# Optimization experiments

Measured on AMD Instinct MI355X. Metric: run time of the kernel, lower is better.

The kernel has to match this reference:

```python
import jax, jax.numpy as jnp
import numpy as np

HEAD_DIM = 128
PATCH = (1, 2, 2)
MAX_SEQ = 1024
THETA = 10000.0
FIXED_REF = 30
H_DIM = 2 * (HEAD_DIM // 6)          # 42
W_DIM = 2 * (HEAD_DIM // 6)          # 42
T_DIM = HEAD_DIM - H_DIM - W_DIM     # 44


def _rope_1d(dim, max_seq_len, theta):
    # matches get_1d_rotary_pos_embed(use_real=True, repeat_interleave_real=True)
    inv = 1.0 / (theta ** (jnp.arange(0, dim, 2, dtype=jnp.float32) / dim))  # [dim/2]
    ang = jnp.arange(max_seq_len, dtype=jnp.float32)[:, None] * inv[None, :]  # [S, dim/2]
    cos = jnp.repeat(jnp.cos(ang), 2, axis=1)  # [S, dim]
    sin = jnp.repeat(jnp.sin(ang), 2, axis=1)
    return cos, sin


def setup_inputs() -> dict:
    key = jax.random.key(0)
    hs = jax.random.normal(key, (1, 16, 22, 120, 120), dtype=jnp.float32)
    t_cos, t_sin = _rope_1d(T_DIM, MAX_SEQ, THETA)
    h_cos, h_sin = _rope_1d(H_DIM, MAX_SEQ, THETA)
    w_cos, w_sin = _rope_1d(W_DIM, MAX_SEQ, THETA)
    return {
        "hidden_states": hs,
        "freq_t_cos": t_cos, "freq_h_cos": h_cos, "freq_w_cos": w_cos,
        "freq_t_sin": t_sin, "freq_h_sin": h_sin, "freq_w_sin": w_sin,
        "num_video_frames": 21,
        "num_ref_frames": 1,
    }


def _build(t_tab, h_tab, w_tab, pos_t, height, width):
    F = pos_t.shape[0]
    t = t_tab[pos_t]                 # [F, T_DIM]
    h = h_tab[:height]               # [height, H_DIM]
    w = w_tab[:width]                # [width, W_DIM]
    grid = jnp.concatenate([
        jnp.broadcast_to(t[:, None, None, :], (F, height, width, T_DIM)),
        jnp.broadcast_to(h[None, :, None, :], (F, height, width, H_DIM)),
        jnp.broadcast_to(w[None, None, :, :], (F, height, width, W_DIM)),
    ], axis=-1)                      # [F, height, width, HEAD_DIM]
    return grid.reshape(1, F * height * width, 1, HEAD_DIM)


def reference(hidden_states, freq_t_cos, freq_h_cos, freq_w_cos,
              freq_t_sin, freq_h_sin, freq_w_sin,
              num_video_frames, num_ref_frames):
    _, _, _, H, W = hidden_states.shape
    p_t, p_h, p_w = PATCH
    height, width = H // p_h, W // p_w
    video_pp = num_video_frames // p_t
    ref_pp = num_ref_frames // p_t
    # temporal positions: sequential for video frames, fixed 30 for ref frames
    pos_t = jnp.concatenate([
        jnp.arange(video_pp, dtype=jnp.int32),
        jnp.full((ref_pp,), FIXED_REF, dtype=jnp.int32),
    ])
    freqs_cos = _build(freq_t_cos, freq_h_cos, freq_w_cos, pos_t, height, width)
    freqs_sin = _build(freq_t_sin, freq_h_sin, freq_w_sin, pos_t, height, width)
    return freqs_cos, freqs_sin
```

## Files before the change

kernel.cpp:

```cpp
#include <hip/hip_runtime.h>


#define RP_T_DIM 44
#define RP_H_DIM 42
#define RP_W_DIM 42
#define RP_HEAD 128
#define RP_GH 60
#define RP_GW 60
#define RP_FIXED_REF 30
#define RP_TH 86
#define RP_TH_PAD 88
#define RP_WROW 44
#define RP_LDS_FLOATS (RP_TH_PAD + RP_GW * RP_WROW)

#define RP_BLOCK 320

__global__ __launch_bounds__(RP_BLOCK) void wan_rope_kernel(
    const float* __restrict__ t_cos, const float* __restrict__ h_cos,
    const float* __restrict__ w_cos, const float* __restrict__ t_sin,
    const float* __restrict__ h_sin, const float* __restrict__ w_sin,
    const int* __restrict__ nvf_ptr,
    float* __restrict__ out, long long sin_offset)
{
    __shared__ __align__(16) float lds_c[RP_LDS_FLOATS];
    __shared__ __align__(16) float lds_s[RP_LDS_FLOATS];

    const int tid = threadIdx.x;
    const int y = blockIdx.x;
    const int f = blockIdx.y;

    const int vpp = nvf_ptr[0];
    const int pos = (f < vpp) ? f : RP_FIXED_REF;

    if (tid < RP_T_DIM) {
        lds_c[tid] = t_cos[pos * RP_T_DIM + tid];
        lds_s[tid] = t_sin[pos * RP_T_DIM + tid];
    } else if (tid < RP_TH) {
        const int j = tid - RP_T_DIM;
        lds_c[tid] = h_cos[y * RP_H_DIM + j];
        lds_s[tid] = h_sin[y * RP_H_DIM + j];
    }

    for (int i = tid; i < 2 * RP_GW; i += RP_BLOCK) {
        const int x = i >> 1, j = i & 1;
        lds_c[RP_TH_PAD + x * RP_WROW + j] = h_cos[y * RP_H_DIM + 40 + j];
        lds_s[RP_TH_PAD + x * RP_WROW + j] = h_sin[y * RP_H_DIM + 40 + j];
    }

    for (int sIdx = tid; sIdx < RP_GW * RP_W_DIM; sIdx += RP_BLOCK) {
        const int x = sIdx / RP_W_DIM;
        const int j = sIdx - x * RP_W_DIM;
        lds_c[RP_TH_PAD + x * RP_WROW + 2 + j] = w_cos[sIdx];
        lds_s[RP_TH_PAD + x * RP_WROW + 2 + j] = w_sin[sIdx];
    }

    __syncthreads();

    const long long rowbase = (long long)f * (RP_GH * RP_GW) + y * RP_GW;
#pragma unroll
    for (int it = 0; it < 6; ++it) {
        const int flat = it * RP_BLOCK + tid;
        const int x = flat >> 5;
        const int q = flat & 31;
        const int lidx = (q < 21) ? (q << 2)
                                  : (RP_TH_PAD + x * RP_WROW + ((q - 21) << 2));
        const float4 c = *(const float4*)(lds_c + lidx);
        const float4 s = *(const float4*)(lds_s + lidx);
        const long long base = (rowbase + x) * RP_HEAD + (q << 2);
        *(float4*)(out + base) = c;
        *(float4*)(out + sin_offset + base) = s;
    }
}

extern "C" void kernel_launch(void* const* d_in, const int* in_sizes, int n_in,
                              void* d_out, int out_size, void* d_ws, size_t ws_size,
                              hipStream_t stream) {
    const float* t_cos = (const float*)d_in[1];
    const float* h_cos = (const float*)d_in[2];
    const float* w_cos = (const float*)d_in[3];
    const float* t_sin = (const float*)d_in[4];
    const float* h_sin = (const float*)d_in[5];
    const float* w_sin = (const float*)d_in[6];
    const int*   nvf   = (const int*)d_in[7];
    float* out = (float*)d_out;

    const long long per_out = (long long)out_size / 2;
    const int F = (int)(per_out / ((long long)RP_GH * RP_GW * RP_HEAD));

    dim3 block(RP_BLOCK);
    dim3 grid(RP_GH, F);
    wan_rope_kernel<<<grid, block, 0, stream>>>(
        t_cos, h_cos, w_cos, t_sin, h_sin, w_sin, nvf, out, per_out);
}
```

Measured before the change: 111.4 us.

## Process four frames per block to reuse staged width tables in LDS

Each block now handles up to four frames for one row instead of one, so the width cos/sin tables staged in shared memory are loaded once and reused across frames. The LDS layout is reorganised into separate regions for per-frame t rows, the shared h row and the w rows, and the store loop precomputes offsets and uses 32-bit indexing. The aim is to cut redundant global loads and per-block setup relative to the write-bound output stream. In exchange the grid has a quarter as many blocks, which may reduce parallelism, and the switch to int offsets assumes the output stays under 2^31 elements.

```diff
diff --git a/kernel.cpp b/kernel.cpp
--- a/kernel.cpp
+++ b/kernel.cpp
@@ -8,67 +8,79 @@
 #define RP_GH 60
 #define RP_GW 60
 #define RP_FIXED_REF 30
-#define RP_TH 86
-#define RP_TH_PAD 88
-#define RP_WROW 44
-#define RP_LDS_FLOATS (RP_TH_PAD + RP_GW * RP_WROW)
+#define RP_FPB 4
+#define RP_BLOCK 320
 
-#define RP_BLOCK 320
+#define RP_HB 176
+#define RP_WB 224
+#define RP_LDSF (RP_WB + RP_GW * 44)
 
 __global__ __launch_bounds__(RP_BLOCK) void wan_rope_kernel(
     const float* __restrict__ t_cos, const float* __restrict__ h_cos,
     const float* __restrict__ w_cos, const float* __restrict__ t_sin,
     const float* __restrict__ h_sin, const float* __restrict__ w_sin,
     const int* __restrict__ nvf_ptr,
-    float* __restrict__ out, long long sin_offset)
+    float* __restrict__ out, int sin_offset, int F)
 {
-    __shared__ __align__(16) float lds_c[RP_LDS_FLOATS];
-    __shared__ __align__(16) float lds_s[RP_LDS_FLOATS];
+    __shared__ __align__(16) float lds_c[RP_LDSF];
+    __shared__ __align__(16) float lds_s[RP_LDSF];
 
     const int tid = threadIdx.x;
-    const int y = blockIdx.x;
-    const int f = blockIdx.y;
+    const int y  = blockIdx.x;
+    const int f0 = blockIdx.y * RP_FPB;
+    const int nf = min(RP_FPB, F - f0);
+    const int vpp = nvf_ptr[0];
 
-    const int vpp = nvf_ptr[0];
-    const int pos = (f < vpp) ? f : RP_FIXED_REF;
-
-    if (tid < RP_T_DIM) {
-        lds_c[tid] = t_cos[pos * RP_T_DIM + tid];
-        lds_s[tid] = t_sin[pos * RP_T_DIM + tid];
-    } else if (tid < RP_TH) {
-        const int j = tid - RP_T_DIM;
-        lds_c[tid] = h_cos[y * RP_H_DIM + j];
-        lds_s[tid] = h_sin[y * RP_H_DIM + j];
+    if (tid < nf * RP_T_DIM) {
+        const int fl = tid / RP_T_DIM;
+        const int d  = tid - fl * RP_T_DIM;
+        const int ff = f0 + fl;
+        const int pos = (ff < vpp) ? ff : RP_FIXED_REF;
+        lds_c[tid] = t_cos[pos * RP_T_DIM + d];
+        lds_s[tid] = t_sin[pos * RP_T_DIM + d];
     }
-
-    for (int i = tid; i < 2 * RP_GW; i += RP_BLOCK) {
-        const int x = i >> 1, j = i & 1;
-        lds_c[RP_TH_PAD + x * RP_WROW + j] = h_cos[y * RP_H_DIM + 40 + j];
-        lds_s[RP_TH_PAD + x * RP_WROW + j] = h_sin[y * RP_H_DIM + 40 + j];
+    if (tid < RP_H_DIM) {
+        lds_c[RP_HB + tid] = h_cos[y * RP_H_DIM + tid];
+        lds_s[RP_HB + tid] = h_sin[y * RP_H_DIM + tid];
     }
-
-    for (int sIdx = tid; sIdx < RP_GW * RP_W_DIM; sIdx += RP_BLOCK) {
-        const int x = sIdx / RP_W_DIM;
-        const int j = sIdx - x * RP_W_DIM;
-        lds_c[RP_TH_PAD + x * RP_WROW + 2 + j] = w_cos[sIdx];
-        lds_s[RP_TH_PAD + x * RP_WROW + 2 + j] = w_sin[sIdx];
+    if (tid < 2 * RP_GW) {
+        const int x = tid >> 1, j = tid & 1;
+        lds_c[RP_WB + x * 44 + j] = h_cos[y * RP_H_DIM + 40 + j];
+        lds_s[RP_WB + x * 44 + j] = h_sin[y * RP_H_DIM + 40 + j];
     }
-
+    for (int i = tid; i < RP_GW * RP_W_DIM; i += RP_BLOCK) {
+        const int x = i / RP_W_DIM;
+        const int j = i - x * RP_W_DIM;
+        lds_c[RP_WB + x * 44 + 2 + j] = w_cos[i];
+        lds_s[RP_WB + x * 44 + 2 + j] = w_sin[i];
+    }
     __syncthreads();
 
-    const long long rowbase = (long long)f * (RP_GH * RP_GW) + y * RP_GW;
+    const int q  = tid & 31;
+    const int xb = tid >> 5;
+
+    const bool is_t = q < 11;
+    const int lidx0 = is_t ? (q << 2)
+                    : ((q < 21) ? (132 + (q << 2))
+                                : (140 + 44 * xb + (q << 2)));
+    const int finc = is_t ? RP_T_DIM : 0;
+    const int winc = (q >= 21) ? 440 : 0;
+
+    int base_f = (f0 * (RP_GH * RP_GW) + y * RP_GW + xb) * RP_HEAD + (q << 2);
+
+    for (int fl = 0; fl < nf; ++fl) {
+        int lidx = lidx0 + fl * finc;
+        int base = base_f;
 #pragma unroll
-    for (int it = 0; it < 6; ++it) {
-        const int flat = it * RP_BLOCK + tid;
-        const int x = flat >> 5;
-        const int q = flat & 31;
-        const int lidx = (q < 21) ? (q << 2)
-                                  : (RP_TH_PAD + x * RP_WROW + ((q - 21) << 2));
-        const float4 c = *(const float4*)(lds_c + lidx);
-        const float4 s = *(const float4*)(lds_s + lidx);
-        const long long base = (rowbase + x) * RP_HEAD + (q << 2);
-        *(float4*)(out + base) = c;
-        *(float4*)(out + sin_offset + base) = s;
+        for (int it = 0; it < 6; ++it) {
+            const float4 c = *(const float4*)(lds_c + lidx);
+            const float4 s = *(const float4*)(lds_s + lidx);
+            *(float4*)(out + base) = c;
+            *(float4*)(out + sin_offset + base) = s;
+            lidx += winc;
+            base += 10 * RP_HEAD;
+        }
+        base_f += RP_GH * RP_GW * RP_HEAD;
     }
 }
 
@@ -84,11 +96,11 @@
     const int*   nvf   = (const int*)d_in[7];
     float* out = (float*)d_out;
 
-    const long long per_out = (long long)out_size / 2;
-    const int F = (int)(per_out / ((long long)RP_GH * RP_GW * RP_HEAD));
+    const int per_out = out_size / 2;
+    const int F = per_out / (RP_GH * RP_GW * RP_HEAD);
 
     dim3 block(RP_BLOCK);
-    dim3 grid(RP_GH, F);
+    dim3 grid(RP_GH, (F + RP_FPB - 1) / RP_FPB);
     wan_rope_kernel<<<grid, block, 0, stream>>>(
-        t_cos, h_cos, w_cos, t_sin, h_sin, w_sin, nvf, out, per_out);
+        t_cos, h_cos, w_cos, t_sin, h_sin, w_sin, nvf, out, per_out, F);
 }
```

Result: no change. 112.2 us (+0.7%).
